# Kernel optimization log

Hardware: AMD Instinct MI355X
Metric: run time of the kernel (lower is better)

Reference implementation:

```python
import jax, jax.numpy as jnp
import numpy as np

N_NODES = 50000
N_EDGES = 800000
N_GRAPHS = 2000
F = 256          # node feature dim == hidden_dim (required by stacked convs)
HID = 256
L = 4
FP = 1034
BN_EPS = 1e-5


def setup_inputs() -> dict:
    key = jax.random.key(0)
    ks = jax.random.split(key, 20)
    s = 0.05
    x = jax.random.normal(ks[0], (N_NODES, F), dtype=jnp.float32)
    edge_index = jax.random.randint(ks[1], (2, N_EDGES), 0, N_NODES, dtype=jnp.int64)
    edge_attr = jax.random.normal(ks[2], (N_EDGES, 1), dtype=jnp.float32)
    fingerprint = jax.random.uniform(ks[3], (N_GRAPHS, FP), dtype=jnp.float32)
    batch = jnp.sort(jax.random.randint(ks[4], (N_NODES,), 0, N_GRAPHS, dtype=jnp.int64))
    # stacked per-layer conv params: message linear [(F+1)->HID], update linear [HID->HID]
    lin_w = jax.random.normal(ks[5], (L, F + 1, HID), dtype=jnp.float32) * s
    lin_b = jax.random.normal(ks[6], (L, HID), dtype=jnp.float32) * s
    upd_w = jax.random.normal(ks[7], (L, HID, HID), dtype=jnp.float32) * s
    upd_b = jax.random.normal(ks[8], (L, HID), dtype=jnp.float32) * s
    # gated-attention pooling gate_nn: Linear(HID,HID) -> tanh -> Linear(HID,1)
    g1_w = jax.random.normal(ks[9], (HID, HID), dtype=jnp.float32) * s
    g1_b = jax.random.normal(ks[10], (HID,), dtype=jnp.float32) * s
    g2_w = jax.random.normal(ks[11], (HID, 1), dtype=jnp.float32) * s
    g2_b = jax.random.normal(ks[12], (1,), dtype=jnp.float32) * s
    fc1_w = jax.random.normal(ks[13], (HID + FP, HID), dtype=jnp.float32) * s
    fc1_b = jax.random.normal(ks[14], (HID,), dtype=jnp.float32) * s
    bn_gamma = jnp.ones((HID,), dtype=jnp.float32)
    bn_beta = jnp.zeros((HID,), dtype=jnp.float32)
    fc2_w = jax.random.normal(ks[15], (HID, 1), dtype=jnp.float32) * s
    fc2_b = jax.random.normal(ks[16], (1,), dtype=jnp.float32) * s
    return dict(x=x, edge_index=edge_index, edge_attr=edge_attr,
                fingerprint=fingerprint, batch=batch,
                lin_w=lin_w, lin_b=lin_b, upd_w=upd_w, upd_b=upd_b,
                g1_w=g1_w, g1_b=g1_b, g2_w=g2_w, g2_b=g2_b,
                fc1_w=fc1_w, fc1_b=fc1_b, bn_gamma=bn_gamma, bn_beta=bn_beta,
                fc2_w=fc2_w, fc2_b=fc2_b)


def reference(x, edge_index, edge_attr, fingerprint, batch,
              lin_w, lin_b, upd_w, upd_b,
              g1_w, g1_b, g2_w, g2_b,
              fc1_w, fc1_b, bn_gamma, bn_beta, fc2_w, fc2_b):
    n = x.shape[0]
    b = fingerprint.shape[0]
    loop = jnp.arange(n, dtype=edge_index.dtype)
    src = jnp.concatenate([edge_index[0], loop])   # x_j = source nodes (PyG default)
    dst = jnp.concatenate([edge_index[1], loop])   # aggregate at target
    ea = jnp.concatenate([edge_attr, jnp.zeros((n, edge_attr.shape[1]), edge_attr.dtype)], axis=0)
    for l in range(L):
        wn, we = lin_w[l, :F], lin_w[l, F:]        # split concat([x_j, edge_attr]) @ W
        msg = jax.nn.relu(x[src] @ wn + ea @ we + lin_b[l])          # [E+n, HID]
        aggr = jax.ops.segment_sum(msg, dst, num_segments=n)          # scatter-add
        x = jax.nn.relu(aggr @ upd_w[l] + upd_b[l])
    # gated attention pooling
    gate = jax.nn.sigmoid(jnp.tanh(x @ g1_w + g1_b) @ g2_w + g2_b)    # [n, 1]
    pooled = jax.ops.segment_sum(x * gate, batch, num_segments=b)     # [b, HID]
    h = jnp.concatenate([pooled, fingerprint], axis=1) @ fc1_w + fc1_b
    # BatchNorm1d (training mode: biased batch stats)
    mu = jnp.mean(h, axis=0)
    var = jnp.mean((h - mu) ** 2, axis=0)
    h = (h - mu) * jax.lax.rsqrt(var + BN_EPS) * bn_gamma + bn_beta
    h = jax.nn.relu(h)  # dropout is identity in eval mode
    return (h @ fc2_w + fc2_b).squeeze(-1)        # [b]
```

## Files before the change

### kernel.cpp

```cpp
#include <hip/hip_runtime.h>
#include <math.h>

#define HIDF 256
#define FPDIM 1034
#define MPAD 50048
#define FCM 2048
#define FCK 1344
#define FCSLICES 3
#define FCKSLICE 448

typedef _Float16 f16x8 __attribute__((ext_vector_type(8)));
typedef _Float16 f16x4 __attribute__((ext_vector_type(4)));
typedef float f32x4 __attribute__((ext_vector_type(4)));

__device__ __forceinline__ float relu_f(float v) { return fmaxf(v, 0.f); }

__global__ __launch_bounds__(256) void convxh_k(
    const float* __restrict__ x, _Float16* __restrict__ xh, int n)
{
    int i = blockIdx.x * 256 + threadIdx.x;
    int row = i >> 6;
    if (row >= MPAD) return;
    f16x4 o;
    if (row < n) {
        float4 v = ((const float4*)x)[i];
        o[0] = (_Float16)v.x; o[1] = (_Float16)v.y;
        o[2] = (_Float16)v.z; o[3] = (_Float16)v.w;
    } else {
        o[0] = o[1] = o[2] = o[3] = (_Float16)0.f;
    }
    ((f16x4*)xh)[i] = o;
}

__global__ __launch_bounds__(256) void convw_all_k(
    const float* __restrict__ lin_w, const float* __restrict__ upd_w,
    const float* __restrict__ g1w, _Float16* __restrict__ whi,
    _Float16* __restrict__ wlo)
{
    int m = blockIdx.y;
    const float* src = (m < 4) ? (lin_w + (size_t)m * 257 * 256)
                     : (m < 8) ? (upd_w + (size_t)(m - 4) * 65536)
                               : g1w;
    int i = blockIdx.x * 256 + threadIdx.x;
    int nn = i >> 8, kk = i & 255;
    float v = src[kk * 256 + nn];
    _Float16 h = (_Float16)v;
    _Float16 l = (_Float16)(v - (float)h);
    whi[(size_t)m * 65536 + i] = h;
    wlo[(size_t)m * 65536 + i] = l;
}

__global__ __launch_bounds__(256) void convfc1a_k(
    const float* __restrict__ pooled, const float* __restrict__ fp,
    _Float16* __restrict__ ahi, _Float16* __restrict__ alo, int B)
{
    int i = blockIdx.x * 256 + threadIdx.x;
    if (i >= FCM * FCK) return;
    int row = i / FCK, col = i - row * FCK;
    float v = 0.f;
    if (row < B) {
        if (col < HIDF) v = pooled[(size_t)row * HIDF + col];
        else if (col < HIDF + FPDIM) v = fp[(size_t)row * FPDIM + (col - HIDF)];
    }
    _Float16 h = (_Float16)v;
    _Float16 l = (_Float16)(v - (float)h);
    ahi[i] = h;
    alo[i] = l;
}

__global__ __launch_bounds__(256) void convfc1w_k(
    const float* __restrict__ w, _Float16* __restrict__ whi,
    _Float16* __restrict__ wlo)
{
    int i = blockIdx.x * 256 + threadIdx.x;
    if (i >= HIDF * FCK) return;
    int nn = i / FCK, kk = i - nn * FCK;
    float v = (kk < HIDF + FPDIM) ? w[(size_t)kk * HIDF + nn] : 0.f;
    _Float16 h = (_Float16)v;
    _Float16 l = (_Float16)(v - (float)h);
    whi[i] = h;
    wlo[i] = l;
}

template <int ACT>
__global__ __launch_bounds__(512) void gemm_f16(
    const _Float16* __restrict__ A, const _Float16* __restrict__ Whi,
    const _Float16* __restrict__ Wlo, const float* __restrict__ bias,
    _Float16* __restrict__ C, int M)
{
    const int N = 256, K = 256;
    __shared__ _Float16 As[128 * 64];
    __shared__ _Float16 Bh[256 * 64];
    __shared__ _Float16 Bl[256 * 64];
    const int tid = threadIdx.x;
    const int wid = tid >> 6, lane = tid & 63;
    const int m0 = blockIdx.y * 128;
    const int wr = wid >> 2, wc = wid & 3;

    f32x4 acc[4][4];
#pragma unroll
    for (int i = 0; i < 4; ++i)
#pragma unroll
        for (int j = 0; j < 4; ++j) acc[i][j] = (f32x4){0.f, 0.f, 0.f, 0.f};

    const int lrow = lane >> 3;
    const int lcol8 = (lane & 7) * 8;

    for (int k0 = 0; k0 < K; k0 += 64) {
#pragma unroll
        for (int i = 0; i < 2; ++i) {
            int iss = wid * 2 + i;
            int row = 8 * iss + lrow;
            const _Float16* ga = A + (size_t)(m0 + row) * K + k0 + lcol8;
            __builtin_amdgcn_global_load_lds(
                (const __attribute__((address_space(1))) void*)ga,
                (__attribute__((address_space(3))) void*)(As + iss * 512), 16, 0, 0);
        }
#pragma unroll
        for (int i = 0; i < 4; ++i) {
            int iss = wid * 4 + i;
            int row = 8 * iss + lrow;
            const _Float16* gh = Whi + (size_t)row * K + k0 + lcol8;
            const _Float16* gl = Wlo + (size_t)row * K + k0 + lcol8;
            __builtin_amdgcn_global_load_lds(
                (const __attribute__((address_space(1))) void*)gh,
                (__attribute__((address_space(3))) void*)(Bh + iss * 512), 16, 0, 0);
            __builtin_amdgcn_global_load_lds(
                (const __attribute__((address_space(1))) void*)gl,
                (__attribute__((address_space(3))) void*)(Bl + iss * 512), 16, 0, 0);
        }
        __syncthreads();
#pragma unroll
        for (int kk = 0; kk < 2; ++kk) {
            const int kb = kk * 32 + (lane >> 4) * 8;
            f16x8 af[4], bh[4], bl[4];
#pragma unroll
            for (int mi = 0; mi < 4; ++mi)
                af[mi] = *(const f16x8*)&As[(wr * 64 + mi * 16 + (lane & 15)) * 64 + kb];
#pragma unroll
            for (int ni = 0; ni < 4; ++ni) {
                int r = (wc * 64 + ni * 16 + (lane & 15)) * 64 + kb;
                bh[ni] = *(const f16x8*)&Bh[r];
                bl[ni] = *(const f16x8*)&Bl[r];
            }
#pragma unroll
            for (int mi = 0; mi < 4; ++mi)
#pragma unroll
                for (int ni = 0; ni < 4; ++ni) {
                    acc[mi][ni] = __builtin_amdgcn_mfma_f32_16x16x32_f16(
                        af[mi], bh[ni], acc[mi][ni], 0, 0, 0);
                    acc[mi][ni] = __builtin_amdgcn_mfma_f32_16x16x32_f16(
                        af[mi], bl[ni], acc[mi][ni], 0, 0, 0);
                }
        }
        __syncthreads();
    }

    const int crow0 = m0 + wr * 64 + (lane >> 4) * 4;
    const int ccol0 = wc * 64 + (lane & 15);
#pragma unroll
    for (int mi = 0; mi < 4; ++mi) {
#pragma unroll
        for (int ni = 0; ni < 4; ++ni) {
            int col = ccol0 + ni * 16;
            float bv = bias ? bias[col] : 0.f;
#pragma unroll
            for (int r = 0; r < 4; ++r) {
                int row = crow0 + mi * 16 + r;
                float v = acc[mi][ni][r] + bv;
                if (ACT == 1) v = relu_f(v);
                else if (ACT == 2) v = tanhf(v);
                C[(size_t)row * N + col] = (_Float16)v;
            }
        }
    }
}

__global__ __launch_bounds__(256) void gemm_fc1(
    const _Float16* __restrict__ Ahi, const _Float16* __restrict__ Alo,
    const _Float16* __restrict__ Whi, const _Float16* __restrict__ Wlo,
    float* __restrict__ C, int Mv, int N, int K)
{
    __shared__ _Float16 Ah[128 * 64];
    __shared__ _Float16 Al[128 * 64];
    __shared__ _Float16 Bh[128 * 64];
    __shared__ _Float16 Bl[128 * 64];
    const int tid = threadIdx.x;
    const int wave = tid >> 6, lane = tid & 63;
    const int m0 = blockIdx.y * 128, n0 = blockIdx.x * 128;
    const int kbeg = blockIdx.z * FCKSLICE;
    const int kend = kbeg + FCKSLICE;
    const int wr = wave >> 1, wc = wave & 1;

    f32x4 acc[4][4];
#pragma unroll
    for (int i = 0; i < 4; ++i)
#pragma unroll
        for (int j = 0; j < 4; ++j) acc[i][j] = (f32x4){0.f, 0.f, 0.f, 0.f};

    const int lrow = lane >> 3;
    const int lcol8 = (lane & 7) * 8;

    for (int k0 = kbeg; k0 < kend; k0 += 64) {
#pragma unroll
        for (int i = 0; i < 4; ++i) {
            int iss = wave * 4 + i;
            int row = 8 * iss + lrow;
            const _Float16* gah = Ahi + (size_t)(m0 + row) * K + k0 + lcol8;
            const _Float16* gal = Alo + (size_t)(m0 + row) * K + k0 + lcol8;
            const _Float16* gbh = Whi + (size_t)(n0 + row) * K + k0 + lcol8;
            const _Float16* gbl = Wlo + (size_t)(n0 + row) * K + k0 + lcol8;
            __builtin_amdgcn_global_load_lds(
                (const __attribute__((address_space(1))) void*)gah,
                (__attribute__((address_space(3))) void*)(Ah + iss * 512), 16, 0, 0);
            __builtin_amdgcn_global_load_lds(
                (const __attribute__((address_space(1))) void*)gal,
                (__attribute__((address_space(3))) void*)(Al + iss * 512), 16, 0, 0);
            __builtin_amdgcn_global_load_lds(
                (const __attribute__((address_space(1))) void*)gbh,
                (__attribute__((address_space(3))) void*)(Bh + iss * 512), 16, 0, 0);
            __builtin_amdgcn_global_load_lds(
                (const __attribute__((address_space(1))) void*)gbl,
                (__attribute__((address_space(3))) void*)(Bl + iss * 512), 16, 0, 0);
        }
        __syncthreads();
#pragma unroll
        for (int kk = 0; kk < 2; ++kk) {
            const int kb = kk * 32 + (lane >> 4) * 8;
            f16x8 ah[4], al[4], bh[4], bl[4];
#pragma unroll
            for (int mi = 0; mi < 4; ++mi) {
                int r = (wr * 64 + mi * 16 + (lane & 15)) * 64 + kb;
                ah[mi] = *(const f16x8*)&Ah[r];
                al[mi] = *(const f16x8*)&Al[r];
            }
#pragma unroll
            for (int ni = 0; ni < 4; ++ni) {
                int r = (wc * 64 + ni * 16 + (lane & 15)) * 64 + kb;
                bh[ni] = *(const f16x8*)&Bh[r];
                bl[ni] = *(const f16x8*)&Bl[r];
            }
#pragma unroll
            for (int mi = 0; mi < 4; ++mi)
#pragma unroll
                for (int ni = 0; ni < 4; ++ni) {
                    acc[mi][ni] = __builtin_amdgcn_mfma_f32_16x16x32_f16(
                        ah[mi], bh[ni], acc[mi][ni], 0, 0, 0);
                    acc[mi][ni] = __builtin_amdgcn_mfma_f32_16x16x32_f16(
                        ah[mi], bl[ni], acc[mi][ni], 0, 0, 0);
                    acc[mi][ni] = __builtin_amdgcn_mfma_f32_16x16x32_f16(
                        al[mi], bh[ni], acc[mi][ni], 0, 0, 0);
                }
        }
        __syncthreads();
    }

    const int crow0 = m0 + wr * 64 + (lane >> 4) * 4;
    const int ccol0 = n0 + wc * 64 + (lane & 15);
#pragma unroll
    for (int mi = 0; mi < 4; ++mi) {
#pragma unroll
        for (int ni = 0; ni < 4; ++ni) {
            int col = ccol0 + ni * 16;
#pragma unroll
            for (int r = 0; r < 4; ++r) {
                int row = crow0 + mi * 16 + r;
                if (row < Mv)
                    atomicAdd(&C[(size_t)row * N + col], acc[mi][ni][r]);
            }
        }
    }
}

__global__ void count_k(const int* __restrict__ dst, int* __restrict__ cnt, int E)
{
    int e = blockIdx.x * blockDim.x + threadIdx.x;
    if (e < E) atomicAdd(&cnt[dst[e]], 1);
}

__global__ __launch_bounds__(256) void scan1_k(
    const int* __restrict__ cnt, int* __restrict__ offs,
    int* __restrict__ bsum, int n)
{
    __shared__ int sh[256];
    int t = threadIdx.x, idx = blockIdx.x * 256 + t;
    int v = (idx < n) ? cnt[idx] : 0;
    sh[t] = v;
    __syncthreads();
    for (int o = 1; o < 256; o <<= 1) {
        int a = (t >= o) ? sh[t - o] : 0;
        __syncthreads();
        sh[t] += a;
        __syncthreads();
    }
    if (idx < n) offs[idx] = sh[t] - v;
    if (t == 255) bsum[blockIdx.x] = sh[255];
}

__global__ __launch_bounds__(256) void scan2_k(int* __restrict__ bsum, int nb)
{
    __shared__ int sh[256];
    int t = threadIdx.x;
    int v = (t < nb) ? bsum[t] : 0;
    sh[t] = v;
    __syncthreads();
    for (int o = 1; o < 256; o <<= 1) {
        int a = (t >= o) ? sh[t - o] : 0;
        __syncthreads();
        sh[t] += a;
        __syncthreads();
    }
    if (t < nb) bsum[t] = sh[t] - v;
}

__global__ __launch_bounds__(256) void scan3_k(
    int* __restrict__ offs, const int* __restrict__ bsum,
    int* __restrict__ cursor, int n, int E)
{
    int idx = blockIdx.x * 256 + threadIdx.x;
    if (idx < n) {
        int o = offs[idx] + bsum[blockIdx.x];
        offs[idx] = o;
        cursor[idx] = o;
    }
    if (idx == 0) offs[n] = E;
}

__global__ void scatter_k(const int* __restrict__ dst, const int* __restrict__ src,
                          const float* __restrict__ ea, int* __restrict__ cursor,
                          int2* __restrict__ esrc, int E)
{
    int e = blockIdx.x * blockDim.x + threadIdx.x;
    if (e < E) {
        int p = atomicAdd(&cursor[dst[e]], 1);
        esrc[p] = make_int2(src[e], __float_as_int(ea[e]));
    }
}

__global__ void start_k(const int* __restrict__ batch, int* __restrict__ start,
                        int n, int B)
{
    int g = blockIdx.x * blockDim.x + threadIdx.x;
    if (g > B) return;
    int lo = 0, hi = n;
    while (lo < hi) {
        int mid = (lo + hi) >> 1;
        if (batch[mid] < g) lo = mid + 1; else hi = mid;
    }
    start[g] = lo;
}

__global__ __launch_bounds__(256) void aggregate_k(
    const _Float16* __restrict__ xw, const float* __restrict__ we,
    const int2* __restrict__ esrc, const int* __restrict__ offs,
    _Float16* __restrict__ out, int n)
{
    int w = (blockIdx.x * blockDim.x + threadIdx.x) >> 6;
    if (w >= n) return;
    const int lane = threadIdx.x & 63;
    const int half = lane >> 5;
    const int f8 = (lane & 31) << 3;

    float we8[8];
    *(float4*)&we8[0] = *(const float4*)(we + f8);
    *(float4*)&we8[4] = *(const float4*)(we + f8 + 4);

    f16x8 xs = *(const f16x8*)(xw + (size_t)w * HIDF + f8);
    float acc[8];
#pragma unroll
    for (int j = 0; j < 8; ++j)
        acc[j] = (half == 0) ? relu_f((float)xs[j]) : 0.f;

    const int e0 = offs[w], e1 = offs[w + 1];
    const int cntE = e1 - e0;
    const int fullPairs = cntE >> 1;

    int t = 0;
    for (; t + 8 <= fullPairs; t += 8) {
        int2 p[8]; f16x8 v[8];
#pragma unroll
        for (int q = 0; q < 8; ++q) p[q] = esrc[e0 + 2 * (t + q) + half];
#pragma unroll
        for (int q = 0; q < 8; ++q)
            v[q] = *(const f16x8*)(xw + (size_t)p[q].x * HIDF + f8);
#pragma unroll
        for (int q = 0; q < 8; ++q) {
            float a = __int_as_float(p[q].y);
#pragma unroll
            for (int j = 0; j < 8; ++j)
                acc[j] += relu_f(fmaf(a, we8[j], (float)v[q][j]));
        }
    }
    for (; t < fullPairs; ++t) {
        int2 p = esrc[e0 + 2 * t + half];
        f16x8 v = *(const f16x8*)(xw + (size_t)p.x * HIDF + f8);
        float a = __int_as_float(p.y);
#pragma unroll
        for (int j = 0; j < 8; ++j)
            acc[j] += relu_f(fmaf(a, we8[j], (float)v[j]));
    }
    if ((cntE & 1) && half == 0) {
        int2 p = esrc[e1 - 1];
        f16x8 v = *(const f16x8*)(xw + (size_t)p.x * HIDF + f8);
        float a = __int_as_float(p.y);
#pragma unroll
        for (int j = 0; j < 8; ++j)
            acc[j] += relu_f(fmaf(a, we8[j], (float)v[j]));
    }

#pragma unroll
    for (int j = 0; j < 8; ++j)
        acc[j] += __shfl_xor(acc[j], 32);

    if (half == 0) {
        f16x8 o;
#pragma unroll
        for (int j = 0; j < 8; ++j) o[j] = (_Float16)acc[j];
        *(f16x8*)(out + (size_t)w * HIDF + f8) = o;
    }
}

__global__ __launch_bounds__(256) void gate_k(
    const _Float16* __restrict__ t, const float* __restrict__ g2w,
    const float* __restrict__ g2b, float* __restrict__ gate, int n)
{
    int w = (blockIdx.x * blockDim.x + threadIdx.x) >> 6;
    if (w >= n) return;
    int lane = threadIdx.x & 63;
    f16x4 tv = *(const f16x4*)(t + (size_t)w * HIDF + (lane << 2));
    float4 g = *(const float4*)(g2w + (lane << 2));
    float s = (float)tv[0] * g.x + (float)tv[1] * g.y
            + (float)tv[2] * g.z + (float)tv[3] * g.w;
    for (int o = 32; o; o >>= 1) s += __shfl_xor(s, o);
    if (lane == 0) gate[w] = 1.f / (1.f + expf(-(s + g2b[0])));
}

__global__ __launch_bounds__(256) void pool_k(
    const _Float16* __restrict__ x, const float* __restrict__ gate,
    const int* __restrict__ start, float* __restrict__ pooled, int B)
{
    int w = (blockIdx.x * blockDim.x + threadIdx.x) >> 6;
    if (w >= B) return;
    int lane = threadIdx.x & 63;
    int f = lane << 2;
    float4 acc = make_float4(0.f, 0.f, 0.f, 0.f);
    int i0 = start[w], i1 = start[w + 1];
    for (int i = i0; i < i1; ++i) {
        float gi = gate[i];
        f16x4 v = *(const f16x4*)(x + (size_t)i * HIDF + f);
        acc.x = fmaf(gi, (float)v[0], acc.x);
        acc.y = fmaf(gi, (float)v[1], acc.y);
        acc.z = fmaf(gi, (float)v[2], acc.z);
        acc.w = fmaf(gi, (float)v[3], acc.w);
    }
    *(float4*)(pooled + (size_t)w * HIDF + f) = acc;
}

__global__ __launch_bounds__(256) void bnstats_k(
    const float* __restrict__ h, const float* __restrict__ fc1b,
    float* __restrict__ mu, float* __restrict__ rs, int B)
{
    int j = blockIdx.x;
    int tid = threadIdx.x;
    float bj = fc1b[j];
    float s = 0.f, s2 = 0.f;
    for (int g = tid; g < B; g += 256) {
        float v = h[(size_t)g * HIDF + j] + bj;
        s += v;
        s2 = fmaf(v, v, s2);
    }
    __shared__ float sh[256], sh2[256];
    sh[tid] = s; sh2[tid] = s2;
    __syncthreads();
    for (int o = 128; o; o >>= 1) {
        if (tid < o) { sh[tid] += sh[tid + o]; sh2[tid] += sh2[tid + o]; }
        __syncthreads();
    }
    if (tid == 0) {
        float m = sh[0] / (float)B;
        float var = sh2[0] / (float)B - m * m;
        if (var < 0.f) var = 0.f;
        mu[j] = m;
        rs[j] = rsqrtf(var + 1e-5f);
    }
}

__global__ __launch_bounds__(256) void final_k(
    const float* __restrict__ h, const float* __restrict__ fc1b,
    const float* __restrict__ mu, const float* __restrict__ rs,
    const float* __restrict__ gamma, const float* __restrict__ beta,
    const float* __restrict__ w2, const float* __restrict__ b2,
    float* __restrict__ out, int B)
{
    int g = blockIdx.x;
    int j = threadIdx.x;
    float v = h[(size_t)g * HIDF + j] + fc1b[j];
    v = (v - mu[j]) * rs[j] * gamma[j] + beta[j];
    v = relu_f(v);
    float term = v * w2[j];
    __shared__ float sh[256];
    sh[j] = term;
    __syncthreads();
    for (int o = 128; o; o >>= 1) {
        if (j < o) sh[j] += sh[j + o];
        __syncthreads();
    }
    if (j == 0) out[g] = sh[0] + b2[0];
}

extern "C" void kernel_launch(void* const* d_in, const int* in_sizes, int n_in,
                              void* d_out, int out_size, void* d_ws, size_t ws_size,
                              hipStream_t stream)
{
    const float* x      = (const float*)d_in[0];
    const int*   ei     = (const int*)d_in[1];
    const float* ea     = (const float*)d_in[2];
    const float* fp     = (const float*)d_in[3];
    const int*   batch  = (const int*)d_in[4];
    const float* lin_w  = (const float*)d_in[5];
    const float* lin_b  = (const float*)d_in[6];
    const float* upd_w  = (const float*)d_in[7];
    const float* upd_b  = (const float*)d_in[8];
    const float* g1w    = (const float*)d_in[9];
    const float* g1b    = (const float*)d_in[10];
    const float* g2w    = (const float*)d_in[11];
    const float* g2b    = (const float*)d_in[12];
    const float* fc1w   = (const float*)d_in[13];
    const float* fc1b   = (const float*)d_in[14];
    const float* gamma  = (const float*)d_in[15];
    const float* beta   = (const float*)d_in[16];
    const float* fc2w   = (const float*)d_in[17];
    const float* fc2b   = (const float*)d_in[18];
    float* out = (float*)d_out;

    const int n = in_sizes[0] / HIDF;
    const int E = in_sizes[1] / 2;
    const int B = in_sizes[3] / FPDIM;
    const int L = in_sizes[5] / (257 * 256);
    const int* srcArr = ei;
    const int* dstArr = ei + E;
    const int nb = (n + 255) / 256;

    char* w = (char*)d_ws;
    _Float16* xh   = (_Float16*)w;  w += (size_t)MPAD * HIDF * 2;
    _Float16* bufA = (_Float16*)w;  w += (size_t)MPAD * HIDF * 2;
    _Float16* bufB = (_Float16*)w;  w += (size_t)MPAD * HIDF * 2;
    _Float16* whi = (_Float16*)w;  w += (size_t)9 * 65536 * 2;
    _Float16* wlo = (_Float16*)w;  w += (size_t)9 * 65536 * 2;
    _Float16* fahi = (_Float16*)w; w += (size_t)FCM * FCK * 2;
    _Float16* falo = (_Float16*)w; w += (size_t)FCM * FCK * 2;
    _Float16* fwhi = (_Float16*)w; w += (size_t)HIDF * FCK * 2;
    _Float16* fwlo = (_Float16*)w; w += (size_t)HIDF * FCK * 2;
    int2*  esrc   = (int2*)w;   w += (size_t)E * 8;
    int*   offs   = (int*)w;    w += ((size_t)n + 4) * 4;
    int*   cursor = (int*)w;    w += ((size_t)n + 4) * 4;
    int*   cnt    = (int*)w;    w += (size_t)n * 4;
    int*   bsum   = (int*)w;    w += 256 * 4;
    int*   startA = (int*)w;    w += ((size_t)B + 4) * 4;
    float* gateA  = (float*)w;  w += (size_t)n * 4;
    float* pooled = (float*)w;  w += (size_t)B * HIDF * 4;
    float* h      = (float*)w;  w += (size_t)B * HIDF * 4;
    float* mu     = (float*)w;  w += 256 * 4;
    float* rs     = (float*)w;  w += 256 * 4;

    hipMemsetAsync(cnt, 0, (size_t)n * 4, stream);
    count_k<<<(E + 255) / 256, 256, 0, stream>>>(dstArr, cnt, E);
    scan1_k<<<nb, 256, 0, stream>>>(cnt, offs, bsum, n);
    scan2_k<<<1, 256, 0, stream>>>(bsum, nb);
    scan3_k<<<nb, 256, 0, stream>>>(offs, bsum, cursor, n, E);
    scatter_k<<<(E + 255) / 256, 256, 0, stream>>>(dstArr, srcArr, ea, cursor, esrc, E);
    start_k<<<(B + 256) / 256, 256, 0, stream>>>(batch, startA, n, B);

    convxh_k<<<(MPAD * 64 + 255) / 256, 256, 0, stream>>>(x, xh, n);
    dim3 gcw(256, 9);
    convw_all_k<<<gcw, 256, 0, stream>>>(lin_w, upd_w, g1w, whi, wlo);
    convfc1w_k<<<(HIDF * FCK + 255) / 256, 256, 0, stream>>>(fc1w, fwhi, fwlo);

    dim3 ggm(1, MPAD / 128);
    for (int l = 0; l < L; ++l) {
        const float* we = lin_w + (size_t)l * 257 * 256 + 256 * 256;
        const float* lb = lin_b + (size_t)l * 256;
        gemm_f16<0><<<ggm, 512, 0, stream>>>(xh, whi + (size_t)l * 65536,
                                             wlo + (size_t)l * 65536, lb, bufA, MPAD);
        aggregate_k<<<(n * 64 + 255) / 256, 256, 0, stream>>>(
            bufA, we, esrc, offs, bufB, n);
        gemm_f16<1><<<ggm, 512, 0, stream>>>(bufB, whi + (size_t)(4 + l) * 65536,
                                             wlo + (size_t)(4 + l) * 65536,
                                             upd_b + (size_t)l * 256, xh, MPAD);
    }

    gemm_f16<2><<<ggm, 512, 0, stream>>>(xh, whi + (size_t)8 * 65536,
                                         wlo + (size_t)8 * 65536, g1b, bufA, MPAD);
    gate_k<<<(n * 64 + 255) / 256, 256, 0, stream>>>(bufA, g2w, g2b, gateA, n);
    pool_k<<<(B * 64 + 255) / 256, 256, 0, stream>>>(xh, gateA, startA, pooled, B);

    convfc1a_k<<<(FCM * FCK + 255) / 256, 256, 0, stream>>>(pooled, fp, fahi, falo, B);
    hipMemsetAsync(h, 0, (size_t)B * HIDF * 4, stream);
    dim3 ggf(HIDF / 128, FCM / 128, FCSLICES);
    gemm_fc1<<<ggf, 256, 0, stream>>>(fahi, falo, fwhi, fwlo, h, B, HIDF, FCK);
    bnstats_k<<<256, 256, 0, stream>>>(h, fc1b, mu, rs, B);
    final_k<<<B, 256, 0, stream>>>(h, fc1b, mu, rs, gamma, beta, fc2w, fc2b, out, B);
}
```

Before: 788.5 us.

## Retile node GEMMs to 128x128 blocks and fuse gate projection into GEMM epilogue

The node GEMMs now use 256-thread blocks with a 128x128 output tile and a 2D grid over N, replacing 512-thread blocks that each computed a full 256-column row tile. This doubles the block count and cuts LDS per block, but A is loaded twice. The gate path is fused: the g1 GEMM epilogue applies tanh, dots with g2w, reduces within the wave, and atomically adds into a per-row accumulator, so the intermediate fp16 tanh matrix is never written. A small kernel then applies the sigmoid. The aggregate kernel's unroll also drops from 8 to 4 edge pairs, which lowers register pressure at the cost of fewer loads in flight.

Result: faster. 671.9 us (-14.8%).

```diff
diff --git a/kernel.cpp b/kernel.cpp
--- a/kernel.cpp
+++ b/kernel.cpp
@@ -83,19 +83,18 @@
 }
 
 template <int ACT>
-__global__ __launch_bounds__(512) void gemm_f16(
+__global__ __launch_bounds__(256) void gemm_f16(
     const _Float16* __restrict__ A, const _Float16* __restrict__ Whi,
     const _Float16* __restrict__ Wlo, const float* __restrict__ bias,
-    _Float16* __restrict__ C, int M)
-{
-    const int N = 256, K = 256;
+    _Float16* __restrict__ C, int M, int N, int K)
+{
     __shared__ _Float16 As[128 * 64];
-    __shared__ _Float16 Bh[256 * 64];
-    __shared__ _Float16 Bl[256 * 64];
+    __shared__ _Float16 Bh[128 * 64];
+    __shared__ _Float16 Bl[128 * 64];
     const int tid = threadIdx.x;
-    const int wid = tid >> 6, lane = tid & 63;
-    const int m0 = blockIdx.y * 128;
-    const int wr = wid >> 2, wc = wid & 3;
+    const int wave = tid >> 6, lane = tid & 63;
+    const int m0 = blockIdx.y * 128, n0 = blockIdx.x * 128;
+    const int wr = wave >> 1, wc = wave & 1;
 
     f32x4 acc[4][4];
 #pragma unroll
@@ -108,20 +107,15 @@
 
     for (int k0 = 0; k0 < K; k0 += 64) {
 #pragma unroll
-        for (int i = 0; i < 2; ++i) {
-            int iss = wid * 2 + i;
+        for (int i = 0; i < 4; ++i) {
+            int iss = wave * 4 + i;
             int row = 8 * iss + lrow;
-            const _Float16* ga = A + (size_t)(m0 + row) * K + k0 + lcol8;
+            const _Float16* ga = A   + (size_t)(m0 + row) * K + k0 + lcol8;
+            const _Float16* gh = Whi + (size_t)(n0 + row) * K + k0 + lcol8;
+            const _Float16* gl = Wlo + (size_t)(n0 + row) * K + k0 + lcol8;
             __builtin_amdgcn_global_load_lds(
                 (const __attribute__((address_space(1))) void*)ga,
                 (__attribute__((address_space(3))) void*)(As + iss * 512), 16, 0, 0);
-        }
-#pragma unroll
-        for (int i = 0; i < 4; ++i) {
-            int iss = wid * 4 + i;
-            int row = 8 * iss + lrow;
-            const _Float16* gh = Whi + (size_t)row * K + k0 + lcol8;
-            const _Float16* gl = Wlo + (size_t)row * K + k0 + lcol8;
             __builtin_amdgcn_global_load_lds(
                 (const __attribute__((address_space(1))) void*)gh,
                 (__attribute__((address_space(3))) void*)(Bh + iss * 512), 16, 0, 0);
@@ -157,7 +151,7 @@
     }
 
     const int crow0 = m0 + wr * 64 + (lane >> 4) * 4;
-    const int ccol0 = wc * 64 + (lane & 15);
+    const int ccol0 = n0 + wc * 64 + (lane & 15);
 #pragma unroll
     for (int mi = 0; mi < 4; ++mi) {
 #pragma unroll
@@ -169,11 +163,122 @@
                 int row = crow0 + mi * 16 + r;
                 float v = acc[mi][ni][r] + bv;
                 if (ACT == 1) v = relu_f(v);
-                else if (ACT == 2) v = tanhf(v);
                 C[(size_t)row * N + col] = (_Float16)v;
             }
         }
     }
+}
+
+__global__ __launch_bounds__(256) void gemm_gate(
+    const _Float16* __restrict__ A, const _Float16* __restrict__ Whi,
+    const _Float16* __restrict__ Wlo, const float* __restrict__ g1b,
+    const float* __restrict__ g2w, float* __restrict__ gacc, int M, int N, int K)
+{
+    __shared__ _Float16 As[128 * 64];
+    __shared__ _Float16 Bh[128 * 64];
+    __shared__ _Float16 Bl[128 * 64];
+    const int tid = threadIdx.x;
+    const int wave = tid >> 6, lane = tid & 63;
+    const int m0 = blockIdx.y * 128, n0 = blockIdx.x * 128;
+    const int wr = wave >> 1, wc = wave & 1;
+
+    f32x4 acc[4][4];
+#pragma unroll
+    for (int i = 0; i < 4; ++i)
+#pragma unroll
+        for (int j = 0; j < 4; ++j) acc[i][j] = (f32x4){0.f, 0.f, 0.f, 0.f};
+
+    const int lrow = lane >> 3;
+    const int lcol8 = (lane & 7) * 8;
+
+    for (int k0 = 0; k0 < K; k0 += 64) {
+#pragma unroll
+        for (int i = 0; i < 4; ++i) {
+            int iss = wave * 4 + i;
+            int row = 8 * iss + lrow;
+            const _Float16* ga = A   + (size_t)(m0 + row) * K + k0 + lcol8;
+            const _Float16* gh = Whi + (size_t)(n0 + row) * K + k0 + lcol8;
+            const _Float16* gl = Wlo + (size_t)(n0 + row) * K + k0 + lcol8;
+            __builtin_amdgcn_global_load_lds(
+                (const __attribute__((address_space(1))) void*)ga,
+                (__attribute__((address_space(3))) void*)(As + iss * 512), 16, 0, 0);
+            __builtin_amdgcn_global_load_lds(
+                (const __attribute__((address_space(1))) void*)gh,
+                (__attribute__((address_space(3))) void*)(Bh + iss * 512), 16, 0, 0);
+            __builtin_amdgcn_global_load_lds(
+                (const __attribute__((address_space(1))) void*)gl,
+                (__attribute__((address_space(3))) void*)(Bl + iss * 512), 16, 0, 0);
+        }
+        __syncthreads();
+#pragma unroll
+        for (int kk = 0; kk < 2; ++kk) {
+            const int kb = kk * 32 + (lane >> 4) * 8;
+            f16x8 af[4], bh[4], bl[4];
+#pragma unroll
+            for (int mi = 0; mi < 4; ++mi)
+                af[mi] = *(const f16x8*)&As[(wr * 64 + mi * 16 + (lane & 15)) * 64 + kb];
+#pragma unroll
+            for (int ni = 0; ni < 4; ++ni) {
+                int r = (wc * 64 + ni * 16 + (lane & 15)) * 64 + kb;
+                bh[ni] = *(const f16x8*)&Bh[r];
+                bl[ni] = *(const f16x8*)&Bl[r];
+            }
+#pragma unroll
+            for (int mi = 0; mi < 4; ++mi)
+#pragma unroll
+                for (int ni = 0; ni < 4; ++ni) {
+                    acc[mi][ni] = __builtin_amdgcn_mfma_f32_16x16x32_f16(
+                        af[mi], bh[ni], acc[mi][ni], 0, 0, 0);
+                    acc[mi][ni] = __builtin_amdgcn_mfma_f32_16x16x32_f16(
+                        af[mi], bl[ni], acc[mi][ni], 0, 0, 0);
+                }
+        }
+        __syncthreads();
+    }
+
+    const int crow0 = m0 + wr * 64 + (lane >> 4) * 4;
+    const int ccol0 = n0 + wc * 64 + (lane & 15);
+    float b1[4], g2[4];
+#pragma unroll
+    for (int ni = 0; ni < 4; ++ni) {
+        b1[ni] = g1b[ccol0 + ni * 16];
+        g2[ni] = g2w[ccol0 + ni * 16];
+    }
+    float p[16];
+#pragma unroll
+    for (int mi = 0; mi < 4; ++mi)
+#pragma unroll
+        for (int r = 0; r < 4; ++r) {
+            float s = 0.f;
+#pragma unroll
+            for (int ni = 0; ni < 4; ++ni) {
+                float v = tanhf(acc[mi][ni][r] + b1[ni]);
+                s = fmaf(v, g2[ni], s);
+            }
+            p[mi * 4 + r] = s;
+        }
+#pragma unroll
+    for (int j = 0; j < 16; ++j) {
+        p[j] += __shfl_xor(p[j], 1);
+        p[j] += __shfl_xor(p[j], 2);
+        p[j] += __shfl_xor(p[j], 4);
+        p[j] += __shfl_xor(p[j], 8);
+    }
+    if ((lane & 15) == 0) {
+#pragma unroll
+        for (int j = 0; j < 16; ++j) {
+            int row = crow0 + (j >> 2) * 16 + (j & 3);
+            atomicAdd(&gacc[row], p[j]);
+        }
+    }
+}
+
+__global__ __launch_bounds__(256) void gatefin_k(
+    const float* __restrict__ gacc, const float* __restrict__ g2b,
+    float* __restrict__ gate, int n)
+{
+    int i = blockIdx.x * 256 + threadIdx.x;
+    if (i < n) gate[i] = 1.f / (1.f + expf(-(gacc[i] + g2b[0])));
 }
 
 __global__ __launch_bounds__(256) void gemm_fc1(
@@ -376,15 +481,15 @@
     const int fullPairs = cntE >> 1;
 
     int t = 0;
-    for (; t + 8 <= fullPairs; t += 8) {
-        int2 p[8]; f16x8 v[8];
-#pragma unroll
-        for (int q = 0; q < 8; ++q) p[q] = esrc[e0 + 2 * (t + q) + half];
-#pragma unroll
-        for (int q = 0; q < 8; ++q)
+    for (; t + 4 <= fullPairs; t += 4) {
+        int2 p[4]; f16x8 v[4];
+#pragma unroll
+        for (int q = 0; q < 4; ++q) p[q] = esrc[e0 + 2 * (t + q) + half];
+#pragma unroll
+        for (int q = 0; q < 4; ++q)
             v[q] = *(const f16x8*)(xw + (size_t)p[q].x * HIDF + f8);
 #pragma unroll
-        for (int q = 0; q < 8; ++q) {
+        for (int q = 0; q < 4; ++q) {
             float a = __int_as_float(p[q].y);
 #pragma unroll
             for (int j = 0; j < 8; ++j)
@@ -418,21 +523,6 @@
         for (int j = 0; j < 8; ++j) o[j] = (_Float16)acc[j];
         *(f16x8*)(out + (size_t)w * HIDF + f8) = o;
     }
-}
-
-__global__ __launch_bounds__(256) void gate_k(
-    const _Float16* __restrict__ t, const float* __restrict__ g2w,
-    const float* __restrict__ g2b, float* __restrict__ gate, int n)
-{
-    int w = (blockIdx.x * blockDim.x + threadIdx.x) >> 6;
-    if (w >= n) return;
-    int lane = threadIdx.x & 63;
-    f16x4 tv = *(const f16x4*)(t + (size_t)w * HIDF + (lane << 2));
-    float4 g = *(const float4*)(g2w + (lane << 2));
-    float s = (float)tv[0] * g.x + (float)tv[1] * g.y
-            + (float)tv[2] * g.z + (float)tv[3] * g.w;
-    for (int o = 32; o; o >>= 1) s += __shfl_xor(s, o);
-    if (lane == 0) gate[w] = 1.f / (1.f + expf(-(s + g2b[0])));
 }
 
 __global__ __launch_bounds__(256) void pool_k(
@@ -558,6 +648,7 @@
     int*   bsum   = (int*)w;    w += 256 * 4;
     int*   startA = (int*)w;    w += ((size_t)B + 4) * 4;
     float* gateA  = (float*)w;  w += (size_t)n * 4;
+    float* gacc   = (float*)w;  w += (size_t)MPAD * 4;
     float* pooled = (float*)w;  w += (size_t)B * HIDF * 4;
     float* h      = (float*)w;  w += (size_t)B * HIDF * 4;
     float* mu     = (float*)w;  w += 256 * 4;
@@ -575,23 +666,26 @@
     dim3 gcw(256, 9);
     convw_all_k<<<gcw, 256, 0, stream>>>(lin_w, upd_w, g1w, whi, wlo);
     convfc1w_k<<<(HIDF * FCK + 255) / 256, 256, 0, stream>>>(fc1w, fwhi, fwlo);
-
-    dim3 ggm(1, MPAD / 128);
+    hipMemsetAsync(gacc, 0, (size_t)MPAD * 4, stream);
+
+    dim3 ggm(HIDF / 128, MPAD / 128);
     for (int l = 0; l < L; ++l) {
         const float* we = lin_w + (size_t)l * 257 * 256 + 256 * 256;
         const float* lb = lin_b + (size_t)l * 256;
-        gemm_f16<0><<<ggm, 512, 0, stream>>>(xh, whi + (size_t)l * 65536,
-                                             wlo + (size_t)l * 65536, lb, bufA, MPAD);
+        gemm_f16<0><<<ggm, 256, 0, stream>>>(xh, whi + (size_t)l * 65536,
+                                             wlo + (size_t)l * 65536, lb,
+                                             bufA, MPAD, HIDF, HIDF);
         aggregate_k<<<(n * 64 + 255) / 256, 256, 0, stream>>>(
             bufA, we, esrc, offs, bufB, n);
-        gemm_f16<1><<<ggm, 512, 0, stream>>>(bufB, whi + (size_t)(4 + l) * 65536,
+        gemm_f16<1><<<ggm, 256, 0, stream>>>(bufB, whi + (size_t)(4 + l) * 65536,
                                              wlo + (size_t)(4 + l) * 65536,
-                                             upd_b + (size_t)l * 256, xh, MPAD);
-    }
-
-    gemm_f16<2><<<ggm, 512, 0, stream>>>(xh, whi + (size_t)8 * 65536,
-                                         wlo + (size_t)8 * 65536, g1b, bufA, MPAD);
-    gate_k<<<(n * 64 + 255) / 256, 256, 0, stream>>>(bufA, g2w, g2b, gateA, n);
+                                             upd_b + (size_t)l * 256, xh, MPAD, HIDF, HIDF);
+    }
+
+    gemm_gate<<<ggm, 256, 0, stream>>>(xh, whi + (size_t)8 * 65536,
+                                       wlo + (size_t)8 * 65536, g1b, g2w,
+                                       gacc, MPAD, HIDF, HIDF);
+    gatefin_k<<<(n + 255) / 256, 256, 0, stream>>>(gacc, g2b, gateA, n);
     pool_k<<<(B * 64 + 255) / 256, 256, 0, stream>>>(xh, gateA, startA, pooled, B);
 
     convfc1a_k<<<(FCM * FCK + 255) / 256, 256, 0, stream>>>(pooled, fp, fahi, falo, B);
```
